# Kernel optimization log

Hardware: AMD Instinct MI355X
Metric: run time of the kernel (lower is better)

## Reference

```python
import jax, jax.numpy as jnp
import numpy as np

GAMMA = 0.997
N_STEPS = 5
EPS = 1e-3
Q_WEIGHTS = np.array([1.0, 0.5, 0.0, 2.0], dtype=np.float32)


def _rescale(x):
    # sign(x) * (sqrt(|x|+1) - 1) + eps * x
    return jnp.sign(x) * (jnp.sqrt(jnp.abs(x) + 1.0) - 1.0) + EPS * x


def _inv_rescale(x):
    sign = jnp.sign(x)
    sqrt_arg = 1.0 + 4.0 * EPS * (jnp.abs(x) + 1.0 + EPS)
    square = ((jnp.sqrt(sqrt_arg) - 1.0) / (2.0 * EPS)) ** 2
    return sign * (square - 1.0)


def setup_inputs() -> dict:
    key = jax.random.key(0)
    ks = jax.random.split(key, 6)
    B, T, Q = 4096, 512, 4
    current_q_value = jax.random.normal(ks[0], (B, T, Q), dtype=jnp.float32)
    next_q_value = jax.random.normal(ks[1], (B, T, Q), dtype=jnp.float32)
    log_p = jax.random.normal(ks[2], (B, T), dtype=jnp.float32)
    reward = jax.random.normal(ks[3], (B, T, Q), dtype=jnp.float32)
    is_done = jax.random.bernoulli(ks[4], 0.02, (B, T)).astype(jnp.float32)
    mask = jax.random.bernoulli(ks[5], 0.95, (B, T)).astype(jnp.float32)
    return {
        "current_q_value": current_q_value,
        "next_q_value": next_q_value,
        "log_p": log_p,
        "reward": reward,
        "is_done": is_done,
        "mask": mask,
    }


def reference(current_q_value, next_q_value, log_p, reward, is_done, mask):
    B, T, Q = reward.shape
    q_w = jnp.asarray(Q_WEIGHTS)[None, None, :]                     # (1,1,Q)
    nz = (q_w != 0)
    inv_qw = jnp.where(nz, 1.0 / jnp.where(nz, q_w, 1.0), 0.0)      # (1,1,Q)
    inv_num_q = 1.0 / float((Q_WEIGHTS != 0).sum())

    m = mask[..., None]                                             # (B,T,1)
    d = is_done[..., None]                                          # (B,T,1)

    nq = m * (1.0 - d) * _inv_rescale(next_q_value)                 # (B,T,Q)
    lp = inv_num_q * inv_qw * (m * (1.0 - d) * log_p[..., None])    # (B,T,Q)

    pad = jnp.zeros((B, N_STEPS - 1, Q), dtype=reward.dtype)
    pad_reward = jnp.concatenate([m * reward, pad], axis=1)         # (B,T+n-1,Q)
    lp_pad = jnp.concatenate([lp, pad], axis=1)                     # (B,T+n-1,Q)

    gpow = GAMMA ** jnp.arange(N_STEPS, dtype=jnp.float32)          # gamma^0..gamma^{n-1}
    widx = jnp.arange(T)[:, None] + jnp.arange(N_STEPS)[None, :]    # (T,n) window indices

    reward_sum = jnp.einsum('btnq,n->btq', pad_reward[:, widx, :], gpow)
    log_p_sum = jnp.einsum('btnq,n->btq', lp_pad[:, widx, :], gpow * GAMMA)

    idxs = jnp.minimum(T - 1, jnp.arange(T) + N_STEPS - 1)          # (T,)
    # NOTE: original code uses gamma**idx (absolute index), reproduced faithfully
    next_term = (GAMMA ** idxs.astype(jnp.float32))[None, :, None] * nq[:, idxs, :]

    target = _rescale(reward_sum + next_term + log_p_sum)           # (B,T,Q)
    loss = 0.5 * m * q_w * (current_q_value - target) ** 2
    return loss
```

## Files before the change

kernel.cpp:

```cpp
#include <hip/hip_runtime.h>
#include <math.h>

#define T_DIM 512
#define GAMMA_F 0.997f
#define EPS_F 1e-3f
#define LOG2_GAMMA (-0.0043345907f)

typedef float v4f __attribute__((ext_vector_type(4)));

__device__ __forceinline__ float inv_rescale_f(float x) {
    float s = (x > 0.f) ? 1.f : ((x < 0.f) ? -1.f : 0.f);
    float sqrt_arg = 1.f + 4.f * EPS_F * (fabsf(x) + 1.f + EPS_F);
    float q = (sqrtf(sqrt_arg) - 1.f) * (1.f / (2.f * EPS_F));
    return s * (q * q - 1.f);
}

__device__ __forceinline__ float rescale_f(float x) {
    return copysignf(sqrtf(fabsf(x) + 1.f) - 1.f, x) + EPS_F * x;
}

__global__ __launch_bounds__(256) void nstep_qloss_kernel(
    const float* __restrict__ cur_q,
    const float* __restrict__ next_q,
    const float* __restrict__ log_p,
    const float* __restrict__ reward,
    const float* __restrict__ is_done,
    const float* __restrict__ mask,
    float* __restrict__ out,
    int BT)
{
    int idx = blockIdx.x * 256 + threadIdx.x;
    if (idx >= BT) return;
    int t = idx & (T_DIM - 1);
    int base = idx - t;

    int s1 = (t + 1 < T_DIM) ? t + 1 : T_DIM - 1;
    int s2 = (t + 2 < T_DIM) ? t + 2 : T_DIM - 1;
    int s3 = (t + 3 < T_DIM) ? t + 3 : T_DIM - 1;
    int s4 = (t + 4 < T_DIM) ? t + 4 : T_DIM - 1;
    int o0 = idx;
    int o1 = base + s1, o2 = base + s2, o3 = base + s3, o4 = base + s4;

    const v4f* rew4 = (const v4f*)reward;
    const v4f* nq4  = (const v4f*)next_q;
    const v4f* cq4  = (const v4f*)cur_q;
    v4f* out4       = (v4f*)out;

    float m0 = mask[o0], m1 = mask[o1], m2 = mask[o2], m3 = mask[o3], m4 = mask[o4];
    float d0 = is_done[o0], d1 = is_done[o1], d2 = is_done[o2], d3 = is_done[o3], d4 = is_done[o4];
    float p0 = log_p[o0], p1 = log_p[o1], p2 = log_p[o2], p3 = log_p[o3], p4 = log_p[o4];
    v4f r0 = rew4[o0], r1 = rew4[o1], r2 = rew4[o2], r3 = rew4[o3], r4 = rew4[o4];
    v4f nq = nq4[o4];
    v4f cq = cq4[o0];
    __builtin_amdgcn_sched_barrier(0);

    float v1 = (t + 1 < T_DIM) ? 1.f : 0.f;
    float v2 = (t + 2 < T_DIM) ? 1.f : 0.f;
    float v3 = (t + 3 < T_DIM) ? 1.f : 0.f;
    float v4v = (t + 4 < T_DIM) ? 1.f : 0.f;

    const float g1 = GAMMA_F;
    const float g2 = g1 * g1;
    const float g3 = g2 * g1;
    const float g4 = g2 * g2;

    float w0 = m0;
    float w1 = v1 * g1 * m1;
    float w2 = v2 * g2 * m2;
    float w3 = v3 * g3 * m3;
    float w4 = v4v * g4 * m4;

    float a0 = w0 * r0.x; float a1 = w0 * r0.y; float a2 = w0 * r0.z; float a3 = w0 * r0.w;
    a0 = fmaf(w1, r1.x, a0); a1 = fmaf(w1, r1.y, a1); a2 = fmaf(w1, r1.z, a2); a3 = fmaf(w1, r1.w, a3);
    a0 = fmaf(w2, r2.x, a0); a1 = fmaf(w2, r2.y, a1); a2 = fmaf(w2, r2.z, a2); a3 = fmaf(w2, r2.w, a3);
    a0 = fmaf(w3, r3.x, a0); a1 = fmaf(w3, r3.y, a1); a2 = fmaf(w3, r3.z, a2); a3 = fmaf(w3, r3.w, a3);
    a0 = fmaf(w4, r4.x, a0); a1 = fmaf(w4, r4.y, a1); a2 = fmaf(w4, r4.z, a2); a3 = fmaf(w4, r4.w, a3);

    float Ls = w0 * (1.f - d0) * p0;
    Ls = fmaf(w1, (1.f - d1) * p1, Ls);
    Ls = fmaf(w2, (1.f - d2) * p2, Ls);
    Ls = fmaf(w3, (1.f - d3) * p3, Ls);
    Ls = fmaf(w4, (1.f - d4) * p4, Ls);
    Ls *= GAMMA_F * (1.f / 3.f);

    float coeff = exp2f((float)s4 * LOG2_GAMMA);
    float g = coeff * m4 * (1.f - d4);
    float nt0 = g * inv_rescale_f(nq.x);
    float nt1 = g * inv_rescale_f(nq.y);
    float nt2 = g * inv_rescale_f(nq.z);
    float nt3 = g * inv_rescale_f(nq.w);

    float tgt0 = rescale_f(a0 + nt0 + 1.0f * Ls);
    float tgt1 = rescale_f(a1 + nt1 + 2.0f * Ls);
    float tgt2 = rescale_f(a2 + nt2);
    float tgt3 = rescale_f(a3 + nt3 + 0.5f * Ls);
    (void)tgt2;

    float hm = 0.5f * m0;
    float e0 = cq.x - tgt0;
    float e1 = cq.y - tgt1;
    float e3 = cq.w - tgt3;
    v4f o;
    o.x = hm * e0 * e0;
    o.y = hm * 0.5f * e1 * e1;
    o.z = 0.f;
    o.w = hm * 2.0f * e3 * e3;
    out4[idx] = o;
}

extern "C" void kernel_launch(void* const* d_in, const int* in_sizes, int n_in,
                              void* d_out, int out_size, void* d_ws, size_t ws_size,
                              hipStream_t stream) {
    const float* cur_q   = (const float*)d_in[0];
    const float* next_q  = (const float*)d_in[1];
    const float* log_p   = (const float*)d_in[2];
    const float* reward  = (const float*)d_in[3];
    const float* is_done = (const float*)d_in[4];
    const float* mask    = (const float*)d_in[5];
    float* out = (float*)d_out;

    int BT = in_sizes[2];
    int blocks = (BT + 255) / 256;
    hipLaunchKernelGGL(nstep_qloss_kernel, dim3(blocks), dim3(256), 0, stream,
                       cur_q, next_q, log_p, reward, is_done, mask, out, BT);
}
```

Baseline: 157.1 us.

## Stage per-row masked rewards and log-probs in shared memory for window reuse

Each block now covers one full T=512 row. Every thread loads its own element once, precomputes the masked reward, masked log-prob and mask*(1-done) into LDS, and then reads the 5-step window from shared memory instead of issuing five overlapping global loads per input. Padding slots at the end of the row replace the per-thread validity tests. The aim is to cut redundant global/L2 traffic and address arithmetic, at the cost of a block-wide barrier and LDS use.

```diff
diff --git a/kernel.cpp b/kernel.cpp
--- a/kernel.cpp
+++ b/kernel.cpp
@@ -19,84 +19,92 @@
     return copysignf(sqrtf(fabsf(x) + 1.f) - 1.f, x) + EPS_F * x;
 }
 
-__global__ __launch_bounds__(256) void nstep_qloss_kernel(
+__global__ __launch_bounds__(512) void nstep_qloss_kernel(
     const float* __restrict__ cur_q,
     const float* __restrict__ next_q,
     const float* __restrict__ log_p,
     const float* __restrict__ reward,
     const float* __restrict__ is_done,
     const float* __restrict__ mask,
-    float* __restrict__ out,
-    int BT)
+    float* __restrict__ out)
 {
-    int idx = blockIdx.x * 256 + threadIdx.x;
-    if (idx >= BT) return;
-    int t = idx & (T_DIM - 1);
-    int base = idx - t;
+    __shared__ v4f   s_mr [T_DIM + 4];
+    __shared__ float s_lpv[T_DIM + 4];
+    __shared__ float s_md [T_DIM + 4];
 
-    int s1 = (t + 1 < T_DIM) ? t + 1 : T_DIM - 1;
-    int s2 = (t + 2 < T_DIM) ? t + 2 : T_DIM - 1;
-    int s3 = (t + 3 < T_DIM) ? t + 3 : T_DIM - 1;
-    int s4 = (t + 4 < T_DIM) ? t + 4 : T_DIM - 1;
-    int o0 = idx;
-    int o1 = base + s1, o2 = base + s2, o3 = base + s3, o4 = base + s4;
+    const int t    = threadIdx.x;
+    const int base = blockIdx.x * T_DIM;
+    const int idx  = base + t;
+    const int s4   = (t + 4 < T_DIM) ? t + 4 : T_DIM - 1;
 
     const v4f* rew4 = (const v4f*)reward;
     const v4f* nq4  = (const v4f*)next_q;
     const v4f* cq4  = (const v4f*)cur_q;
-    v4f* out4       = (v4f*)out;
+    v4f*       out4 = (v4f*)out;
 
-    float m0 = mask[o0], m1 = mask[o1], m2 = mask[o2], m3 = mask[o3], m4 = mask[o4];
-    float d0 = is_done[o0], d1 = is_done[o1], d2 = is_done[o2], d3 = is_done[o3], d4 = is_done[o4];
-    float p0 = log_p[o0], p1 = log_p[o1], p2 = log_p[o2], p3 = log_p[o3], p4 = log_p[o4];
-    v4f r0 = rew4[o0], r1 = rew4[o1], r2 = rew4[o2], r3 = rew4[o3], r4 = rew4[o4];
-    v4f nq = nq4[o4];
-    v4f cq = cq4[o0];
-    __builtin_amdgcn_sched_barrier(0);
+    float m = mask[idx];
+    float d = is_done[idx];
+    float p = log_p[idx];
+    v4f   r = rew4[idx];
+    v4f  nq = nq4[base + s4];
+    v4f  cq = cq4[idx];
 
-    float v1 = (t + 1 < T_DIM) ? 1.f : 0.f;
-    float v2 = (t + 2 < T_DIM) ? 1.f : 0.f;
-    float v3 = (t + 3 < T_DIM) ? 1.f : 0.f;
-    float v4v = (t + 4 < T_DIM) ? 1.f : 0.f;
+    float md = m * (1.f - d);
+    s_mr [t] = m * r;
+    s_lpv[t] = md * p;
+    s_md [t] = md;
+    if (t == T_DIM - 1) {
+        v4f z; z.x = 0.f; z.y = 0.f; z.z = 0.f; z.w = 0.f;
+        #pragma unroll
+        for (int k = 1; k <= 4; ++k) {
+            s_mr [T_DIM - 1 + k] = z;
+            s_lpv[T_DIM - 1 + k] = 0.f;
+            s_md [T_DIM - 1 + k] = md;
+        }
+    }
+    __syncthreads();
 
     const float g1 = GAMMA_F;
     const float g2 = g1 * g1;
     const float g3 = g2 * g1;
     const float g4 = g2 * g2;
 
-    float w0 = m0;
-    float w1 = v1 * g1 * m1;
-    float w2 = v2 * g2 * m2;
-    float w3 = v3 * g3 * m3;
-    float w4 = v4v * g4 * m4;
+    v4f A0 = s_mr[t];
+    v4f A1 = s_mr[t + 1];
+    v4f A2 = s_mr[t + 2];
+    v4f A3 = s_mr[t + 3];
+    v4f A4 = s_mr[t + 4];
+    float l0 = s_lpv[t];
+    float l1 = s_lpv[t + 1];
+    float l2 = s_lpv[t + 2];
+    float l3 = s_lpv[t + 3];
+    float l4 = s_lpv[t + 4];
+    float md4 = s_md[t + 4];
 
-    float a0 = w0 * r0.x; float a1 = w0 * r0.y; float a2 = w0 * r0.z; float a3 = w0 * r0.w;
-    a0 = fmaf(w1, r1.x, a0); a1 = fmaf(w1, r1.y, a1); a2 = fmaf(w1, r1.z, a2); a3 = fmaf(w1, r1.w, a3);
-    a0 = fmaf(w2, r2.x, a0); a1 = fmaf(w2, r2.y, a1); a2 = fmaf(w2, r2.z, a2); a3 = fmaf(w2, r2.w, a3);
-    a0 = fmaf(w3, r3.x, a0); a1 = fmaf(w3, r3.y, a1); a2 = fmaf(w3, r3.z, a2); a3 = fmaf(w3, r3.w, a3);
-    a0 = fmaf(w4, r4.x, a0); a1 = fmaf(w4, r4.y, a1); a2 = fmaf(w4, r4.z, a2); a3 = fmaf(w4, r4.w, a3);
+    float a0 = A0.x, a1 = A0.y, a3 = A0.w;
+    a0 = fmaf(g1, A1.x, a0); a1 = fmaf(g1, A1.y, a1); a3 = fmaf(g1, A1.w, a3);
+    a0 = fmaf(g2, A2.x, a0); a1 = fmaf(g2, A2.y, a1); a3 = fmaf(g2, A2.w, a3);
+    a0 = fmaf(g3, A3.x, a0); a1 = fmaf(g3, A3.y, a1); a3 = fmaf(g3, A3.w, a3);
+    a0 = fmaf(g4, A4.x, a0); a1 = fmaf(g4, A4.y, a1); a3 = fmaf(g4, A4.w, a3);
 
-    float Ls = w0 * (1.f - d0) * p0;
-    Ls = fmaf(w1, (1.f - d1) * p1, Ls);
-    Ls = fmaf(w2, (1.f - d2) * p2, Ls);
-    Ls = fmaf(w3, (1.f - d3) * p3, Ls);
-    Ls = fmaf(w4, (1.f - d4) * p4, Ls);
+    float Ls = l0;
+    Ls = fmaf(g1, l1, Ls);
+    Ls = fmaf(g2, l2, Ls);
+    Ls = fmaf(g3, l3, Ls);
+    Ls = fmaf(g4, l4, Ls);
     Ls *= GAMMA_F * (1.f / 3.f);
 
     float coeff = exp2f((float)s4 * LOG2_GAMMA);
-    float g = coeff * m4 * (1.f - d4);
+    float g = coeff * md4;
     float nt0 = g * inv_rescale_f(nq.x);
     float nt1 = g * inv_rescale_f(nq.y);
-    float nt2 = g * inv_rescale_f(nq.z);
     float nt3 = g * inv_rescale_f(nq.w);
 
     float tgt0 = rescale_f(a0 + nt0 + 1.0f * Ls);
     float tgt1 = rescale_f(a1 + nt1 + 2.0f * Ls);
-    float tgt2 = rescale_f(a2 + nt2);
     float tgt3 = rescale_f(a3 + nt3 + 0.5f * Ls);
-    (void)tgt2;
 
-    float hm = 0.5f * m0;
+    float hm = 0.5f * m;
     float e0 = cq.x - tgt0;
     float e1 = cq.y - tgt1;
     float e3 = cq.w - tgt3;
@@ -120,7 +128,7 @@
     float* out = (float*)d_out;
 
     int BT = in_sizes[2];
-    int blocks = (BT + 255) / 256;
-    hipLaunchKernelGGL(nstep_qloss_kernel, dim3(blocks), dim3(256), 0, stream,
-                       cur_q, next_q, log_p, reward, is_done, mask, out, BT);
+    int blocks = BT / T_DIM;
+    hipLaunchKernelGGL(nstep_qloss_kernel, dim3(blocks), dim3(512), 0, stream,
+                       cur_q, next_q, log_p, reward, is_done, mask, out);
 }
```

Result: no change. 159.6 us (+1.6%).

## Process four timesteps per thread to reuse window loads in registers

Applied to the files above, without the earlier changes.

Each thread now handles four consecutive timesteps, reusing the overlapping 5-step reward, mask and log_p window from registers instead of reloading it per timestep. Scalar mask, done and log_p loads become vector loads, and the unused z component of the reward sum is dropped. This cuts redundant load instructions and cache traffic. In exchange there are four times fewer threads, higher register pressure and strided per-thread access for the 16-byte reward and q loads, which can hurt coalescing.

```diff
diff --git a/kernel.cpp b/kernel.cpp
--- a/kernel.cpp
+++ b/kernel.cpp
@@ -29,83 +29,140 @@
     float* __restrict__ out,
     int BT)
 {
-    int idx = blockIdx.x * 256 + threadIdx.x;
-    if (idx >= BT) return;
-    int t = idx & (T_DIM - 1);
-    int base = idx - t;
+    const int cid = blockIdx.x * 256 + threadIdx.x;
+    if (cid * 4 >= BT) return;
+    const int b    = cid >> 7;
+    const int t0   = (cid & 127) << 2;
+    const int base = b * T_DIM;
 
-    int s1 = (t + 1 < T_DIM) ? t + 1 : T_DIM - 1;
-    int s2 = (t + 2 < T_DIM) ? t + 2 : T_DIM - 1;
-    int s3 = (t + 3 < T_DIM) ? t + 3 : T_DIM - 1;
-    int s4 = (t + 4 < T_DIM) ? t + 4 : T_DIM - 1;
-    int o0 = idx;
-    int o1 = base + s1, o2 = base + s2, o3 = base + s3, o4 = base + s4;
+    const int h4 = (t0 + 4 < T_DIM) ? t0 + 4 : T_DIM - 1;
+    const int h5 = (t0 + 5 < T_DIM) ? t0 + 5 : T_DIM - 1;
+    const int h6 = (t0 + 6 < T_DIM) ? t0 + 6 : T_DIM - 1;
+    const int h7 = (t0 + 7 < T_DIM) ? t0 + 7 : T_DIM - 1;
+    const float va4 = (t0 + 4 < T_DIM) ? 1.f : 0.f;
+    const float va5 = (t0 + 5 < T_DIM) ? 1.f : 0.f;
+    const float va6 = (t0 + 6 < T_DIM) ? 1.f : 0.f;
+    const float va7 = (t0 + 7 < T_DIM) ? 1.f : 0.f;
 
     const v4f* rew4 = (const v4f*)reward;
     const v4f* nq4  = (const v4f*)next_q;
     const v4f* cq4  = (const v4f*)cur_q;
-    v4f* out4       = (v4f*)out;
+    v4f*       out4 = (v4f*)out;
 
-    float m0 = mask[o0], m1 = mask[o1], m2 = mask[o2], m3 = mask[o3], m4 = mask[o4];
-    float d0 = is_done[o0], d1 = is_done[o1], d2 = is_done[o2], d3 = is_done[o3], d4 = is_done[o4];
-    float p0 = log_p[o0], p1 = log_p[o1], p2 = log_p[o2], p3 = log_p[o3], p4 = log_p[o4];
-    v4f r0 = rew4[o0], r1 = rew4[o1], r2 = rew4[o2], r3 = rew4[o3], r4 = rew4[o4];
-    v4f nq = nq4[o4];
-    v4f cq = cq4[o0];
-    __builtin_amdgcn_sched_barrier(0);
+    v4f m_o = *(const v4f*)(mask    + base + t0);
+    v4f d_o = *(const v4f*)(is_done + base + t0);
+    v4f p_o = *(const v4f*)(log_p   + base + t0);
+    float mh4 = mask[base + h4], mh5 = mask[base + h5], mh6 = mask[base + h6], mh7 = mask[base + h7];
+    float dh4 = is_done[base + h4], dh5 = is_done[base + h5], dh6 = is_done[base + h6], dh7 = is_done[base + h7];
+    float ph4 = log_p[base + h4], ph5 = log_p[base + h5], ph6 = log_p[base + h6], ph7 = log_p[base + h7];
+    v4f r0 = rew4[base + t0];
+    v4f r1 = rew4[base + t0 + 1];
+    v4f r2 = rew4[base + t0 + 2];
+    v4f r3 = rew4[base + t0 + 3];
+    v4f r4 = rew4[base + h4];
+    v4f r5 = rew4[base + h5];
+    v4f r6 = rew4[base + h6];
+    v4f r7 = rew4[base + h7];
+    v4f n0 = nq4[base + h4];
+    v4f n1 = nq4[base + h5];
+    v4f n2 = nq4[base + h6];
+    v4f n3 = nq4[base + h7];
+    v4f c0 = cq4[base + t0];
+    v4f c1 = cq4[base + t0 + 1];
+    v4f c2 = cq4[base + t0 + 2];
+    v4f c3 = cq4[base + t0 + 3];
 
-    float v1 = (t + 1 < T_DIM) ? 1.f : 0.f;
-    float v2 = (t + 2 < T_DIM) ? 1.f : 0.f;
-    float v3 = (t + 3 < T_DIM) ? 1.f : 0.f;
-    float v4v = (t + 4 < T_DIM) ? 1.f : 0.f;
+    float md4 = mh4 * (1.f - dh4);
+    float md5 = mh5 * (1.f - dh5);
+    float md6 = mh6 * (1.f - dh6);
+    float md7 = mh7 * (1.f - dh7);
+    float lz0 = m_o.x * (1.f - d_o.x) * p_o.x;
+    float lz1 = m_o.y * (1.f - d_o.y) * p_o.y;
+    float lz2 = m_o.z * (1.f - d_o.z) * p_o.z;
+    float lz3 = m_o.w * (1.f - d_o.w) * p_o.w;
+    float lz4 = va4 * md4 * ph4;
+    float lz5 = va5 * md5 * ph5;
+    float lz6 = va6 * md6 * ph6;
+    float lz7 = va7 * md7 * ph7;
+    float w0 = m_o.x, w1 = m_o.y, w2 = m_o.z, w3 = m_o.w;
+    float w4 = va4 * mh4, w5 = va5 * mh5, w6 = va6 * mh6, w7 = va7 * mh7;
+    float x0 = w0 * r0.x, y0 = w0 * r0.y, z0 = w0 * r0.w;
+    float x1 = w1 * r1.x, y1 = w1 * r1.y, z1 = w1 * r1.w;
+    float x2 = w2 * r2.x, y2 = w2 * r2.y, z2 = w2 * r2.w;
+    float x3 = w3 * r3.x, y3 = w3 * r3.y, z3 = w3 * r3.w;
+    float x4 = w4 * r4.x, y4 = w4 * r4.y, z4 = w4 * r4.w;
+    float x5 = w5 * r5.x, y5 = w5 * r5.y, z5 = w5 * r5.w;
+    float x6 = w6 * r6.x, y6 = w6 * r6.y, z6 = w6 * r6.w;
+    float x7 = w7 * r7.x, y7 = w7 * r7.y, z7 = w7 * r7.w;
 
     const float g1 = GAMMA_F;
     const float g2 = g1 * g1;
     const float g3 = g2 * g1;
     const float g4 = g2 * g2;
+    const float LSC = GAMMA_F * (1.f / 3.f);
 
-    float w0 = m0;
-    float w1 = v1 * g1 * m1;
-    float w2 = v2 * g2 * m2;
-    float w3 = v3 * g3 * m3;
-    float w4 = v4v * g4 * m4;
+    float a0 = x0; a0 = fmaf(g1, x1, a0); a0 = fmaf(g2, x2, a0); a0 = fmaf(g3, x3, a0); a0 = fmaf(g4, x4, a0);
+    float b0 = y0; b0 = fmaf(g1, y1, b0); b0 = fmaf(g2, y2, b0); b0 = fmaf(g3, y3, b0); b0 = fmaf(g4, y4, b0);
+    float e0 = z0; e0 = fmaf(g1, z1, e0); e0 = fmaf(g2, z2, e0); e0 = fmaf(g3, z3, e0); e0 = fmaf(g4, z4, e0);
+    float L0 = lz0; L0 = fmaf(g1, lz1, L0); L0 = fmaf(g2, lz2, L0); L0 = fmaf(g3, lz3, L0); L0 = fmaf(g4, lz4, L0);
+    L0 *= LSC;
+    float a1 = x1; a1 = fmaf(g1, x2, a1); a1 = fmaf(g2, x3, a1); a1 = fmaf(g3, x4, a1); a1 = fmaf(g4, x5, a1);
+    float b1 = y1; b1 = fmaf(g1, y2, b1); b1 = fmaf(g2, y3, b1); b1 = fmaf(g3, y4, b1); b1 = fmaf(g4, y5, b1);
+    float e1 = z1; e1 = fmaf(g1, z2, e1); e1 = fmaf(g2, z3, e1); e1 = fmaf(g3, z4, e1); e1 = fmaf(g4, z5, e1);
+    float L1 = lz1; L1 = fmaf(g1, lz2, L1); L1 = fmaf(g2, lz3, L1); L1 = fmaf(g3, lz4, L1); L1 = fmaf(g4, lz5, L1);
+    L1 *= LSC;
+    float a2 = x2; a2 = fmaf(g1, x3, a2); a2 = fmaf(g2, x4, a2); a2 = fmaf(g3, x5, a2); a2 = fmaf(g4, x6, a2);
+    float b2 = y2; b2 = fmaf(g1, y3, b2); b2 = fmaf(g2, y4, b2); b2 = fmaf(g3, y5, b2); b2 = fmaf(g4, y6, b2);
+    float e2 = z2; e2 = fmaf(g1, z3, e2); e2 = fmaf(g2, z4, e2); e2 = fmaf(g3, z5, e2); e2 = fmaf(g4, z6, e2);
+    float L2 = lz2; L2 = fmaf(g1, lz3, L2); L2 = fmaf(g2, lz4, L2); L2 = fmaf(g3, lz5, L2); L2 = fmaf(g4, lz6, L2);
+    L2 *= LSC;
+    float a3 = x3; a3 = fmaf(g1, x4, a3); a3 = fmaf(g2, x5, a3); a3 = fmaf(g3, x6, a3); a3 = fmaf(g4, x7, a3);
+    float b3 = y3; b3 = fmaf(g1, y4, b3); b3 = fmaf(g2, y5, b3); b3 = fmaf(g3, y6, b3); b3 = fmaf(g4, y7, b3);
+    float e3 = z3; e3 = fmaf(g1, z4, e3); e3 = fmaf(g2, z5, e3); e3 = fmaf(g3, z6, e3); e3 = fmaf(g4, z7, e3);
+    float L3 = lz3; L3 = fmaf(g1, lz4, L3); L3 = fmaf(g2, lz5, L3); L3 = fmaf(g3, lz6, L3); L3 = fmaf(g4, lz7, L3);
+    L3 *= LSC;
 
-    float a0 = w0 * r0.x; float a1 = w0 * r0.y; float a2 = w0 * r0.z; float a3 = w0 * r0.w;
-    a0 = fmaf(w1, r1.x, a0); a1 = fmaf(w1, r1.y, a1); a2 = fmaf(w1, r1.z, a2); a3 = fmaf(w1, r1.w, a3);
-    a0 = fmaf(w2, r2.x, a0); a1 = fmaf(w2, r2.y, a1); a2 = fmaf(w2, r2.z, a2); a3 = fmaf(w2, r2.w, a3);
-    a0 = fmaf(w3, r3.x, a0); a1 = fmaf(w3, r3.y, a1); a2 = fmaf(w3, r3.z, a2); a3 = fmaf(w3, r3.w, a3);
-    a0 = fmaf(w4, r4.x, a0); a1 = fmaf(w4, r4.y, a1); a2 = fmaf(w4, r4.z, a2); a3 = fmaf(w4, r4.w, a3);
+    float q0 = exp2f((float)h4 * LOG2_GAMMA) * md4;
+    float q1 = exp2f((float)h5 * LOG2_GAMMA) * md5;
+    float q2 = exp2f((float)h6 * LOG2_GAMMA) * md6;
+    float q3 = exp2f((float)h7 * LOG2_GAMMA) * md7;
 
-    float Ls = w0 * (1.f - d0) * p0;
-    Ls = fmaf(w1, (1.f - d1) * p1, Ls);
-    Ls = fmaf(w2, (1.f - d2) * p2, Ls);
-    Ls = fmaf(w3, (1.f - d3) * p3, Ls);
-    Ls = fmaf(w4, (1.f - d4) * p4, Ls);
-    Ls *= GAMMA_F * (1.f / 3.f);
-
-    float coeff = exp2f((float)s4 * LOG2_GAMMA);
-    float g = coeff * m4 * (1.f - d4);
-    float nt0 = g * inv_rescale_f(nq.x);
-    float nt1 = g * inv_rescale_f(nq.y);
-    float nt2 = g * inv_rescale_f(nq.z);
-    float nt3 = g * inv_rescale_f(nq.w);
-
-    float tgt0 = rescale_f(a0 + nt0 + 1.0f * Ls);
-    float tgt1 = rescale_f(a1 + nt1 + 2.0f * Ls);
-    float tgt2 = rescale_f(a2 + nt2);
-    float tgt3 = rescale_f(a3 + nt3 + 0.5f * Ls);
-    (void)tgt2;
-
-    float hm = 0.5f * m0;
-    float e0 = cq.x - tgt0;
-    float e1 = cq.y - tgt1;
-    float e3 = cq.w - tgt3;
-    v4f o;
-    o.x = hm * e0 * e0;
-    o.y = hm * 0.5f * e1 * e1;
-    o.z = 0.f;
-    o.w = hm * 2.0f * e3 * e3;
-    out4[idx] = o;
+    {
+        float t0x = rescale_f(a0 + q0 * inv_rescale_f(n0.x) + 1.0f * L0);
+        float t0y = rescale_f(b0 + q0 * inv_rescale_f(n0.y) + 2.0f * L0);
+        float t0w = rescale_f(e0 + q0 * inv_rescale_f(n0.w) + 0.5f * L0);
+        float hm = 0.5f * m_o.x;
+        float u0 = c0.x - t0x, u1 = c0.y - t0y, u3 = c0.w - t0w;
+        v4f o; o.x = hm * u0 * u0; o.y = hm * 0.5f * u1 * u1; o.z = 0.f; o.w = hm * 2.0f * u3 * u3;
+        out4[base + t0] = o;
+    }
+    {
+        float t1x = rescale_f(a1 + q1 * inv_rescale_f(n1.x) + 1.0f * L1);
+        float t1y = rescale_f(b1 + q1 * inv_rescale_f(n1.y) + 2.0f * L1);
+        float t1w = rescale_f(e1 + q1 * inv_rescale_f(n1.w) + 0.5f * L1);
+        float hm = 0.5f * m_o.y;
+        float u0 = c1.x - t1x, u1 = c1.y - t1y, u3 = c1.w - t1w;
+        v4f o; o.x = hm * u0 * u0; o.y = hm * 0.5f * u1 * u1; o.z = 0.f; o.w = hm * 2.0f * u3 * u3;
+        out4[base + t0 + 1] = o;
+    }
+    {
+        float t2x = rescale_f(a2 + q2 * inv_rescale_f(n2.x) + 1.0f * L2);
+        float t2y = rescale_f(b2 + q2 * inv_rescale_f(n2.y) + 2.0f * L2);
+        float t2w = rescale_f(e2 + q2 * inv_rescale_f(n2.w) + 0.5f * L2);
+        float hm = 0.5f * m_o.z;
+        float u0 = c2.x - t2x, u1 = c2.y - t2y, u3 = c2.w - t2w;
+        v4f o; o.x = hm * u0 * u0; o.y = hm * 0.5f * u1 * u1; o.z = 0.f; o.w = hm * 2.0f * u3 * u3;
+        out4[base + t0 + 2] = o;
+    }
+    {
+        float t3x = rescale_f(a3 + q3 * inv_rescale_f(n3.x) + 1.0f * L3);
+        float t3y = rescale_f(b3 + q3 * inv_rescale_f(n3.y) + 2.0f * L3);
+        float t3w = rescale_f(e3 + q3 * inv_rescale_f(n3.w) + 0.5f * L3);
+        float hm = 0.5f * m_o.w;
+        float u0 = c3.x - t3x, u1 = c3.y - t3y, u3 = c3.w - t3w;
+        v4f o; o.x = hm * u0 * u0; o.y = hm * 0.5f * u1 * u1; o.z = 0.f; o.w = hm * 2.0f * u3 * u3;
+        out4[base + t0 + 3] = o;
+    }
 }
 
 extern "C" void kernel_launch(void* const* d_in, const int* in_sizes, int n_in,
@@ -120,7 +177,8 @@
     float* out = (float*)d_out;
 
     int BT = in_sizes[2];
-    int blocks = (BT + 255) / 256;
+    int chunks = BT / 4;
+    int blocks = (chunks + 255) / 256;
     hipLaunchKernelGGL(nstep_qloss_kernel, dim3(blocks), dim3(256), 0, stream,
                        cur_q, next_q, log_p, reward, is_done, mask, out, BT);
 }
```

Measured after the change: 177.5 us. 13.0% more time.

## Use persistent wave tasks with shuffle halo sharing and double-buffered loads

Applied to the files above, without the earlier changes.

Switches to a persistent grid of 1024 blocks. Each wavefront works through tasks of 60 useful timesteps plus a 4-lane halo, and loads for the next task are issued before computing the current one (software double-buffering). Mask, done and log_p for the neighbour timesteps now come from wavefront shuffles instead of four extra scalar loads each, which cuts redundant scalar load traffic. In exchange about 6% of lanes compute halo results that are thrown away, and the 64-lane tasks with a 60 stride give misaligned, partly overlapping vector loads.

```diff
diff --git a/kernel.cpp b/kernel.cpp
--- a/kernel.cpp
+++ b/kernel.cpp
@@ -5,6 +5,10 @@
 #define GAMMA_F 0.997f
 #define EPS_F 1e-3f
 #define LOG2_GAMMA (-0.0043345907f)
+#define WIDTH 60
+#define TASKS_PER_ROW 9
+#define NBLOCKS 1024
+#define TPB 256
 
 typedef float v4f __attribute__((ext_vector_type(4)));
 
@@ -27,85 +31,125 @@
     const float* __restrict__ is_done,
     const float* __restrict__ mask,
     float* __restrict__ out,
-    int BT)
+    int nrows)
 {
-    int idx = blockIdx.x * 256 + threadIdx.x;
-    if (idx >= BT) return;
-    int t = idx & (T_DIM - 1);
-    int base = idx - t;
-
-    int s1 = (t + 1 < T_DIM) ? t + 1 : T_DIM - 1;
-    int s2 = (t + 2 < T_DIM) ? t + 2 : T_DIM - 1;
-    int s3 = (t + 3 < T_DIM) ? t + 3 : T_DIM - 1;
-    int s4 = (t + 4 < T_DIM) ? t + 4 : T_DIM - 1;
-    int o0 = idx;
-    int o1 = base + s1, o2 = base + s2, o3 = base + s3, o4 = base + s4;
+    const int lane = threadIdx.x & 63;
+    const int wid  = (blockIdx.x << 2) + (threadIdx.x >> 6);
+    const int NW   = gridDim.x << 2;
+    const int total = nrows * TASKS_PER_ROW;
+    const int nj = (wid < total) ? ((total - 1 - wid) / NW + 1) : 0;
+    if (nj == 0) return;
 
     const v4f* rew4 = (const v4f*)reward;
     const v4f* nq4  = (const v4f*)next_q;
     const v4f* cq4  = (const v4f*)cur_q;
-    v4f* out4       = (v4f*)out;
-
-    float m0 = mask[o0], m1 = mask[o1], m2 = mask[o2], m3 = mask[o3], m4 = mask[o4];
-    float d0 = is_done[o0], d1 = is_done[o1], d2 = is_done[o2], d3 = is_done[o3], d4 = is_done[o4];
-    float p0 = log_p[o0], p1 = log_p[o1], p2 = log_p[o2], p3 = log_p[o3], p4 = log_p[o4];
-    v4f r0 = rew4[o0], r1 = rew4[o1], r2 = rew4[o2], r3 = rew4[o3], r4 = rew4[o4];
-    v4f nq = nq4[o4];
-    v4f cq = cq4[o0];
-    __builtin_amdgcn_sched_barrier(0);
-
-    float v1 = (t + 1 < T_DIM) ? 1.f : 0.f;
-    float v2 = (t + 2 < T_DIM) ? 1.f : 0.f;
-    float v3 = (t + 3 < T_DIM) ? 1.f : 0.f;
-    float v4v = (t + 4 < T_DIM) ? 1.f : 0.f;
+    v4f*       out4 = (v4f*)out;
 
     const float g1 = GAMMA_F;
     const float g2 = g1 * g1;
     const float g3 = g2 * g1;
     const float g4 = g2 * g2;
+    const float LSC = GAMMA_F * (1.f / 3.f);
 
-    float w0 = m0;
-    float w1 = v1 * g1 * m1;
-    float w2 = v2 * g2 * m2;
-    float w3 = v3 * g3 * m3;
-    float w4 = v4v * g4 * m4;
+    float mA, dA, pA, mB, dB, pB;
+    v4f r0A, r1A, r2A, r3A, r4A, nqA, cqA;
+    v4f r0B, r1B, r2B, r3B, r4B, nqB, cqB;
 
-    float a0 = w0 * r0.x; float a1 = w0 * r0.y; float a2 = w0 * r0.z; float a3 = w0 * r0.w;
-    a0 = fmaf(w1, r1.x, a0); a1 = fmaf(w1, r1.y, a1); a2 = fmaf(w1, r1.z, a2); a3 = fmaf(w1, r1.w, a3);
-    a0 = fmaf(w2, r2.x, a0); a1 = fmaf(w2, r2.y, a1); a2 = fmaf(w2, r2.z, a2); a3 = fmaf(w2, r2.w, a3);
-    a0 = fmaf(w3, r3.x, a0); a1 = fmaf(w3, r3.y, a1); a2 = fmaf(w3, r3.z, a2); a3 = fmaf(w3, r3.w, a3);
-    a0 = fmaf(w4, r4.x, a0); a1 = fmaf(w4, r4.y, a1); a2 = fmaf(w4, r4.z, a2); a3 = fmaf(w4, r4.w, a3);
+#define LOADK(S, TK) do {                                                   \
+    int row_ = (TK) / TASKS_PER_ROW;                                        \
+    int sub_ = (TK) - row_ * TASKS_PER_ROW;                                 \
+    int tt_  = sub_ * WIDTH + lane;                                         \
+    int b_   = row_ * T_DIM;                                                \
+    int tl_  = (tt_     < T_DIM) ? tt_     : T_DIM - 1;                     \
+    int h1_  = (tt_ + 1 < T_DIM) ? tt_ + 1 : T_DIM - 1;                     \
+    int h2_  = (tt_ + 2 < T_DIM) ? tt_ + 2 : T_DIM - 1;                     \
+    int h3_  = (tt_ + 3 < T_DIM) ? tt_ + 3 : T_DIM - 1;                     \
+    int h4_  = (tt_ + 4 < T_DIM) ? tt_ + 4 : T_DIM - 1;                     \
+    m##S  = mask[b_ + tl_];                                                 \
+    d##S  = is_done[b_ + tl_];                                              \
+    p##S  = log_p[b_ + tl_];                                                \
+    r0##S = rew4[b_ + tl_];                                                 \
+    r1##S = rew4[b_ + h1_];                                                 \
+    r2##S = rew4[b_ + h2_];                                                 \
+    r3##S = rew4[b_ + h3_];                                                 \
+    r4##S = rew4[b_ + h4_];                                                 \
+    nq##S = nq4 [b_ + h4_];                                                 \
+    cq##S = cq4 [b_ + tl_];                                                 \
+} while (0)
 
-    float Ls = w0 * (1.f - d0) * p0;
-    Ls = fmaf(w1, (1.f - d1) * p1, Ls);
-    Ls = fmaf(w2, (1.f - d2) * p2, Ls);
-    Ls = fmaf(w3, (1.f - d3) * p3, Ls);
-    Ls = fmaf(w4, (1.f - d4) * p4, Ls);
-    Ls *= GAMMA_F * (1.f / 3.f);
+#define COMPUTEK(S, TK) do {                                                \
+    int row_ = (TK) / TASKS_PER_ROW;                                        \
+    int sub_ = (TK) - row_ * TASKS_PER_ROW;                                 \
+    int tt_  = sub_ * WIDTH + lane;                                         \
+    int b_   = row_ * T_DIM;                                                \
+    int s4_  = (tt_ + 4 < T_DIM) ? tt_ + 4 : T_DIM - 1;                     \
+    float v1_ = (tt_ + 1 < T_DIM) ? 1.f : 0.f;                              \
+    float v2_ = (tt_ + 2 < T_DIM) ? 1.f : 0.f;                              \
+    float v3_ = (tt_ + 3 < T_DIM) ? 1.f : 0.f;                              \
+    float v4_ = (tt_ + 4 < T_DIM) ? 1.f : 0.f;                              \
+    float MD_ = m##S * (1.f - d##S);                                        \
+    float LZ_ = MD_ * p##S;                                                 \
+    float M1_ = __shfl_down(m##S, 1);                                       \
+    float M2_ = __shfl_down(m##S, 2);                                       \
+    float M3_ = __shfl_down(m##S, 3);                                       \
+    float M4_ = __shfl_down(m##S, 4);                                       \
+    float L1_ = __shfl_down(LZ_, 1);                                        \
+    float L2_ = __shfl_down(LZ_, 2);                                        \
+    float L3_ = __shfl_down(LZ_, 3);                                        \
+    float L4_ = __shfl_down(LZ_, 4);                                        \
+    float MD4_ = __shfl_down(MD_, 4);                                       \
+    float w0_ = m##S;                                                       \
+    float w1_ = v1_ * g1 * M1_;                                             \
+    float w2_ = v2_ * g2 * M2_;                                             \
+    float w3_ = v3_ * g3 * M3_;                                             \
+    float w4_ = v4_ * g4 * M4_;                                             \
+    float a0_ = w0_ * r0##S.x, a1_ = w0_ * r0##S.y, a3_ = w0_ * r0##S.w;    \
+    a0_ = fmaf(w1_, r1##S.x, a0_); a1_ = fmaf(w1_, r1##S.y, a1_); a3_ = fmaf(w1_, r1##S.w, a3_); \
+    a0_ = fmaf(w2_, r2##S.x, a0_); a1_ = fmaf(w2_, r2##S.y, a1_); a3_ = fmaf(w2_, r2##S.w, a3_); \
+    a0_ = fmaf(w3_, r3##S.x, a0_); a1_ = fmaf(w3_, r3##S.y, a1_); a3_ = fmaf(w3_, r3##S.w, a3_); \
+    a0_ = fmaf(w4_, r4##S.x, a0_); a1_ = fmaf(w4_, r4##S.y, a1_); a3_ = fmaf(w4_, r4##S.w, a3_); \
+    float Ls_ = LZ_;                                                        \
+    Ls_ = fmaf(v1_ * g1, L1_, Ls_);                                         \
+    Ls_ = fmaf(v2_ * g2, L2_, Ls_);                                         \
+    Ls_ = fmaf(v3_ * g3, L3_, Ls_);                                         \
+    Ls_ = fmaf(v4_ * g4, L4_, Ls_);                                         \
+    Ls_ *= LSC;                                                             \
+    float coeff_ = exp2f((float)s4_ * LOG2_GAMMA);                          \
+    float gg_ = coeff_ * MD4_;                                              \
+    float nt0_ = gg_ * inv_rescale_f(nq##S.x);                              \
+    float nt1_ = gg_ * inv_rescale_f(nq##S.y);                              \
+    float nt3_ = gg_ * inv_rescale_f(nq##S.w);                              \
+    float tgt0_ = rescale_f(a0_ + nt0_ + 1.0f * Ls_);                       \
+    float tgt1_ = rescale_f(a1_ + nt1_ + 2.0f * Ls_);                       \
+    float tgt3_ = rescale_f(a3_ + nt3_ + 0.5f * Ls_);                       \
+    float hm_ = 0.5f * m##S;                                                \
+    float e0_ = cq##S.x - tgt0_;                                            \
+    float e1_ = cq##S.y - tgt1_;                                            \
+    float e3_ = cq##S.w - tgt3_;                                            \
+    v4f o_;                                                                 \
+    o_.x = hm_ * e0_ * e0_;                                                 \
+    o_.y = hm_ * 0.5f * e1_ * e1_;                                          \
+    o_.z = 0.f;                                                             \
+    o_.w = hm_ * 2.0f * e3_ * e3_;                                          \
+    if (lane < WIDTH && tt_ < T_DIM) out4[b_ + tt_] = o_;                   \
+} while (0)
 
-    float coeff = exp2f((float)s4 * LOG2_GAMMA);
-    float g = coeff * m4 * (1.f - d4);
-    float nt0 = g * inv_rescale_f(nq.x);
-    float nt1 = g * inv_rescale_f(nq.y);
-    float nt2 = g * inv_rescale_f(nq.z);
-    float nt3 = g * inv_rescale_f(nq.w);
-
-    float tgt0 = rescale_f(a0 + nt0 + 1.0f * Ls);
-    float tgt1 = rescale_f(a1 + nt1 + 2.0f * Ls);
-    float tgt2 = rescale_f(a2 + nt2);
-    float tgt3 = rescale_f(a3 + nt3 + 0.5f * Ls);
-    (void)tgt2;
-
-    float hm = 0.5f * m0;
-    float e0 = cq.x - tgt0;
-    float e1 = cq.y - tgt1;
-    float e3 = cq.w - tgt3;
-    v4f o;
-    o.x = hm * e0 * e0;
-    o.y = hm * 0.5f * e1 * e1;
-    o.z = 0.f;
-    o.w = hm * 2.0f * e3 * e3;
-    out4[idx] = o;
+    int k = 0;
+    LOADK(A, wid);
+    for (;;) {
+        int tk = wid + k * NW;
+        if (k + 1 < nj) LOADK(B, tk + NW);
+        __builtin_amdgcn_sched_barrier(0);
+        COMPUTEK(A, tk);
+        if (++k >= nj) break;
+        tk = wid + k * NW;
+        if (k + 1 < nj) LOADK(A, tk + NW);
+        __builtin_amdgcn_sched_barrier(0);
+        COMPUTEK(B, tk);
+        if (++k >= nj) break;
+    }
+#undef LOADK
+#undef COMPUTEK
 }
 
 extern "C" void kernel_launch(void* const* d_in, const int* in_sizes, int n_in,
@@ -120,7 +164,7 @@
     float* out = (float*)d_out;
 
     int BT = in_sizes[2];
-    int blocks = (BT + 255) / 256;
-    hipLaunchKernelGGL(nstep_qloss_kernel, dim3(blocks), dim3(256), 0, stream,
-                       cur_q, next_q, log_p, reward, is_done, mask, out, BT);
+    int nrows = BT / T_DIM;
+    hipLaunchKernelGGL(nstep_qloss_kernel, dim3(NBLOCKS), dim3(TPB), 0, stream,
+                       cur_q, next_q, log_p, reward, is_done, mask, out, nrows);
 }
```

Result: slower. 162.9 us (+3.7%).
